# Optimization experiments

Hardware: AMD Instinct MI355X
Metric: run time of the kernel (lower is better)

The kernel has to match this reference:

```python
import jax, jax.numpy as jnp
import numpy as np

B, C, H, W = 8, 256, 64, 64
GROUPS = 32
EPS = 1e-5


def setup_inputs() -> dict:
    key = jax.random.key(0)
    ks = jax.random.split(key, 6)
    s = 1.0 / np.sqrt(C)
    return {
        "x": jax.random.normal(ks[0], (B, C, H, W), dtype=jnp.float32),
        "gn_w": jnp.ones((C,), jnp.float32),
        "gn_b": jnp.zeros((C,), jnp.float32),
        "wq": jax.random.normal(ks[1], (C, C), jnp.float32) * s,
        "bq": jnp.zeros((C,), jnp.float32),
        "wk": jax.random.normal(ks[2], (C, C), jnp.float32) * s,
        "bk": jnp.zeros((C,), jnp.float32),
        "wv": jax.random.normal(ks[3], (C, C), jnp.float32) * s,
        "bv": jnp.zeros((C,), jnp.float32),
        "wo": jax.random.normal(ks[4], (C, C), jnp.float32) * s,
        "bo": jnp.zeros((C,), jnp.float32),
    }


def group_norm(x, w, b):
    # x: [B, C, H, W]; normalize over (C//GROUPS, H, W) per group
    Bn, Cn, Hn, Wn = x.shape
    xg = x.reshape(Bn, GROUPS, Cn // GROUPS, Hn, Wn)
    mu = jnp.mean(xg, axis=(2, 3, 4), keepdims=True)
    var = jnp.var(xg, axis=(2, 3, 4), keepdims=True)
    xn = (xg - mu) * jax.lax.rsqrt(var + EPS)
    xn = xn.reshape(Bn, Cn, Hn, Wn)
    return xn * w[None, :, None, None] + b[None, :, None, None]


def reference(x, gn_w, gn_b, wq, bq, wk, bk, wv, bv, wo, bo):
    Bn, Cn, Hn, Wn = x.shape
    h = group_norm(x, gn_w, gn_b)
    hf = h.reshape(Bn, Cn, Hn * Wn)  # [B, C, N]
    # 1x1 conv == channel matmul; produce tokens-major [B, N, C]
    q = jnp.einsum('bcn,oc->bno', hf, wq) + bq  # [B, N, C]
    k = jnp.einsum('bcn,oc->bon', hf, wk) + bk[None, :, None]  # [B, C, N]
    v = jnp.einsum('bcn,oc->bno', hf, wv) + bv  # [B, N, C]
    alpha = jnp.einsum('bnc,bcm->bnm', q, k) / jnp.sqrt(jnp.float32(Cn))
    alpha = jax.nn.softmax(alpha, axis=-1)  # [B, N, N]
    out = jnp.einsum('bnm,bmc->bnc', alpha, v)  # [B, N, C]
    out = jnp.einsum('bnc,oc->bon', out, wo) + bo[None, :, None]  # [B, C, N]
    return out.reshape(Bn, Cn, Hn, Wn) + x
```

## Files before the change

kernel.cpp:

```cpp
#include <hip/hip_runtime.h>
#include <hip/hip_bf16.h>
#include <cstdint>


typedef short short8 __attribute__((ext_vector_type(8)));
typedef float f32x16 __attribute__((ext_vector_type(16)));

__device__ __forceinline__ unsigned short f2bf(float f){
  uint32_t u = __builtin_bit_cast(uint32_t, f);
  u += 0x7FFFu + ((u >> 16) & 1u);
  return (unsigned short)(u >> 16);
}
__device__ __forceinline__ uint32_t pk2t(float a, float b){
  return (__builtin_bit_cast(uint32_t,a)>>16) | (__builtin_bit_cast(uint32_t,b)&0xFFFF0000u);
}
__device__ __forceinline__ void gload16(const void* g, void* l){
  auto gp = reinterpret_cast<uint32_t __attribute__((address_space(1)))*>(
      reinterpret_cast<uintptr_t>(g));
  auto lp = reinterpret_cast<uint32_t __attribute__((address_space(3)))*>(
      reinterpret_cast<uintptr_t>(l));
  __builtin_amdgcn_global_load_lds(gp, lp, 16, 0, 0);
}

__global__ void cvt_w_kernel(const float* wq, const float* wk, const float* wv, const float* wo,
                             ushort* wqb, ushort* wkb, ushort* wvb, ushort* wob){
  int i = blockIdx.x*256 + threadIdx.x;
  wqb[i]=f2bf(wq[i]); wkb[i]=f2bf(wk[i]); wvb[i]=f2bf(wv[i]); wob[i]=f2bf(wo[i]);
}

__global__ void gn_stats_kernel(const float* __restrict__ x, float* __restrict__ gst){
  int bg = blockIdx.x;
  const float* p = x + (size_t)bg*32768;
  float s=0.f, sq=0.f;
  for(int i=threadIdx.x;i<32768;i+=256){ float v=p[i]; s+=v; sq+=v*v; }
  #pragma unroll
  for(int o=32;o>0;o>>=1){ s+=__shfl_down(s,o); sq+=__shfl_down(sq,o); }
  __shared__ float ls[4], lq[4];
  if((threadIdx.x&63)==0){ ls[threadIdx.x>>6]=s; lq[threadIdx.x>>6]=sq; }
  __syncthreads();
  if(threadIdx.x==0){
    s=ls[0]+ls[1]+ls[2]+ls[3]; sq=lq[0]+lq[1]+lq[2]+lq[3];
    float mu=s*(1.f/32768.f);
    float var=sq*(1.f/32768.f)-mu*mu;
    gst[bg*2]=mu; gst[bg*2+1]=rsqrtf(var+1e-5f);
  }
}

__global__ void gn_apply_kernel(const float* __restrict__ x, const float* __restrict__ gw,
                                const float* __restrict__ gb, const float* __restrict__ gst,
                                ushort* __restrict__ ht){
  int nt=blockIdx.x, ct=blockIdx.y, b=blockIdx.z;
  int n0=nt*64, c0=ct*32;
  __shared__ float tile[32][65];
  __shared__ float smu[4], srs[4], sw[32], sb[32];
  int tid=threadIdx.x;
  if(tid<4){ int g=(c0>>3)+tid; smu[tid]=gst[(b*32+g)*2]; srs[tid]=gst[(b*32+g)*2+1]; }
  if(tid<32){ sw[tid]=gw[c0+tid]; sb[tid]=gb[c0+tid]; }
  __syncthreads();
  int ci=tid>>3, j0=(tid&7)*8;
  const float* xp = x + ((size_t)(b*256)+c0+ci)*4096 + n0 + j0;
  float mu=smu[ci>>3], rs=srs[ci>>3], w=sw[ci], bb=sb[ci];
  #pragma unroll
  for(int j=0;j<8;j++){ tile[ci][j0+j]=(xp[j]-mu)*rs*w+bb; }
  __syncthreads();
  int nl=tid>>2, oct=tid&3;
  union{ ushort u[8]; uint4 v; } o;
  #pragma unroll
  for(int j=0;j<8;j++) o.u[j]=f2bf(tile[oct*8+j][nl]);
  *reinterpret_cast<uint4*>(ht + ((size_t)(b*4096)+n0+nl)*256 + c0 + oct*8) = o.v;
}

__global__ __launch_bounds__(256,2) void gemm_qk(const ushort* __restrict__ A,
         const ushort* __restrict__ Bq, const ushort* __restrict__ Bk,
         ushort* __restrict__ Dq, ushort* __restrict__ Dk,
         const float* __restrict__ bq, const float* __restrict__ bk, float qscale){
  __shared__ ushort Al[128*64];
  __shared__ ushort Bql[128*64];
  __shared__ ushort Bkl[128*64];
  int m0=blockIdx.x*128, n0=blockIdx.y*128;
  int tid=threadIdx.x, w=tid>>6, lane=tid&63, ln=lane&31, hi=lane>>5;
  f32x16 aq[2][2], ak[2][2];
  #pragma unroll
  for(int a=0;a<2;a++)
    #pragma unroll
    for(int c=0;c<2;c++)
      #pragma unroll
      for(int r=0;r<16;r++){ aq[a][c][r]=0.f; ak[a][c][r]=0.f; }
  for(int kt=0;kt<4;kt++){
    __syncthreads();
    #pragma unroll
    for(int i=0;i<4;i++){
      int idx=i*256+tid; int row=idx>>3; int chs=(idx^row)&7;
      gload16(A  + (size_t)(m0+row)*256 + kt*64 + chs*8, (char*)Al  + (i*256+w*64)*16);
    }
    #pragma unroll
    for(int i=0;i<4;i++){
      int idx=i*256+tid; int row=idx>>3; int chs=(idx^row)&7;
      gload16(Bq + (size_t)(n0+row)*256 + kt*64 + chs*8, (char*)Bql + (i*256+w*64)*16);
    }
    #pragma unroll
    for(int i=0;i<4;i++){
      int idx=i*256+tid; int row=idx>>3; int chs=(idx^row)&7;
      gload16(Bk + (size_t)(n0+row)*256 + kt*64 + chs*8, (char*)Bkl + (i*256+w*64)*16);
    }
    __syncthreads();
    #pragma unroll
    for(int kk=0;kk<4;kk++){
      short8 af[2], bqf[2], bkf[2];
      #pragma unroll
      for(int t=0;t<2;t++){
        int ra=(w>>1)*64+t*32+ln; int ca=((kk*2+hi)^ra)&7;
        af[t]=*reinterpret_cast<const short8*>(Al + ra*64 + ca*8);
        int rb=(w&1)*64+t*32+ln; int cb=((kk*2+hi)^rb)&7;
        bqf[t]=*reinterpret_cast<const short8*>(Bql + rb*64 + cb*8);
        bkf[t]=*reinterpret_cast<const short8*>(Bkl + rb*64 + cb*8);
      }
      #pragma unroll
      for(int ti=0;ti<2;ti++)
        #pragma unroll
        for(int tj=0;tj<2;tj++){
          aq[ti][tj]=__builtin_amdgcn_mfma_f32_32x32x16_bf16(af[ti],bqf[tj],aq[ti][tj],0,0,0);
          ak[ti][tj]=__builtin_amdgcn_mfma_f32_32x32x16_bf16(af[ti],bkf[tj],ak[ti][tj],0,0,0);
        }
    }
  }
  #pragma unroll
  for(int ti=0;ti<2;ti++){
    #pragma unroll
    for(int tj=0;tj<2;tj++){
      int col=n0+(w&1)*64+tj*32+ln;
      float bqc=bq[col], bkc=bk[col];
      #pragma unroll
      for(int r=0;r<16;r++){
        int row=m0+(w>>1)*64+ti*32+(r&3)+8*(r>>2)+4*hi;
        Dq[(size_t)row*256+col]=f2bf((aq[ti][tj][r]+bqc)*qscale);
        Dk[(size_t)row*256+col]=f2bf(ak[ti][tj][r]+bkc);
      }
    }
  }
}

__global__ __launch_bounds__(256,2) void gemm_vt(const ushort* __restrict__ A, const ushort* __restrict__ Bm,
         ushort* __restrict__ D, const float* __restrict__ bias){
  __shared__ ushort Al[128*64];
  __shared__ ushort Bl[128*64];
  int m0=blockIdx.x*128, n0=blockIdx.y*128;
  int tid=threadIdx.x, w=tid>>6, lane=tid&63, ln=lane&31, hi=lane>>5;
  f32x16 acc[2][2];
  #pragma unroll
  for(int a=0;a<2;a++)
    #pragma unroll
    for(int c=0;c<2;c++)
      #pragma unroll
      for(int r=0;r<16;r++) acc[a][c][r]=0.f;
  for(int kt=0;kt<4;kt++){
    __syncthreads();
    #pragma unroll
    for(int i=0;i<4;i++){
      int idx=i*256+tid; int row=idx>>3; int chs=(idx^row)&7;
      gload16(A + (size_t)(m0+row)*256 + kt*64 + chs*8, (char*)Al + (i*256+w*64)*16);
    }
    #pragma unroll
    for(int i=0;i<4;i++){
      int idx=i*256+tid; int row=idx>>3; int chs=(idx^row)&7;
      gload16(Bm + (size_t)(n0+row)*256 + kt*64 + chs*8, (char*)Bl + (i*256+w*64)*16);
    }
    __syncthreads();
    #pragma unroll
    for(int kk=0;kk<4;kk++){
      short8 af[2], bfr[2];
      #pragma unroll
      for(int t=0;t<2;t++){
        int ra=(w>>1)*64+t*32+ln; int ca=((kk*2+hi)^ra)&7;
        af[t]=*reinterpret_cast<const short8*>(Al + ra*64 + ca*8);
        int rb=(w&1)*64+t*32+ln; int cb=((kk*2+hi)^rb)&7;
        bfr[t]=*reinterpret_cast<const short8*>(Bl + rb*64 + cb*8);
      }
      #pragma unroll
      for(int ti=0;ti<2;ti++)
        #pragma unroll
        for(int tj=0;tj<2;tj++)
          acc[ti][tj]=__builtin_amdgcn_mfma_f32_32x32x16_bf16(af[ti],bfr[tj],acc[ti][tj],0,0,0);
    }
  }
  #pragma unroll
  for(int ti=0;ti<2;ti++){
    #pragma unroll
    for(int tj=0;tj<2;tj++){
      int col=n0+(w&1)*64+tj*32+ln;
      #pragma unroll
      for(int r=0;r<16;r++){
        int row=m0+(w>>1)*64+ti*32+(r&3)+8*(r>>2)+4*hi;
        D[(size_t)row*32768+col]=f2bf(acc[ti][tj][r]+bias[row]);
      }
    }
  }
}

__global__ __launch_bounds__(512,2) void attn_kernel(
    const ushort* __restrict__ qb, const ushort* __restrict__ kb,
    const ushort* __restrict__ vtb, const ushort* __restrict__ wob,
    const float* __restrict__ bo, const float* __restrict__ x,
    float* __restrict__ out){
  __shared__ ushort smem[2][32768];
  __shared__ float ml[8][2][32];
  float* exch = reinterpret_cast<float*>(&smem[0][0]);
  int tid=threadIdx.x, w=tid>>6, lane=tid&63, ln=lane&31, hi=lane>>5;
  int qg=w&3, h=w>>2;
  int b=blockIdx.y, n0=blockIdx.x*128+qg*32;
  int n=n0+ln;
  short8 qf[16];
  {
    const ushort* qrow = qb + ((size_t)(b*4096)+n)*256 + hi*8;
    #pragma unroll
    for(int kc=0;kc<16;kc++) qf[kc]=*reinterpret_cast<const short8*>(qrow+kc*16);
  }
  f32x16 oacc[8];
  #pragma unroll
  for(int i=0;i<8;i++)
    #pragma unroll
    for(int r=0;r<16;r++) oacc[i][r]=0.f;
  float M=-3.0e38f, L=0.f;
  const ushort* kbp = kb + (size_t)b*4096*256;
  const ushort* vbp = vtb + (size_t)b*4096;

  auto stage=[&](int t1, int bufi){
    char* Kd=(char*)&smem[bufi][0];
    char* Vd=(char*)&smem[bufi][16384];
    #pragma unroll
    for(int i=0;i<4;i++){
      int idx=i*512+tid; int row=idx>>5, ch=idx&31;
      int chs=(ch&24)|((ch^row)&7);
      gload16(kbp + (size_t)(t1*64+row)*256 + chs*8, Kd + (i*512+w*64)*16);
    }
    #pragma unroll
    for(int i=0;i<4;i++){
      int idx=i*512+tid; int row=idx>>3; int chs=(idx^row)&7;
      gload16(vbp + (size_t)row*32768 + t1*64 + chs*8, Vd + (i*512+w*64)*16);
    }
  };

  stage(0, 0);

  for(int t=0;t<64;t++){
    int cur=t&1;
    if(t<63){
      stage(t+1, cur^1);
      asm volatile("s_waitcnt vmcnt(8)" ::: "memory");
    } else {
      asm volatile("s_waitcnt vmcnt(0)" ::: "memory");
    }
    asm volatile("s_barrier" ::: "memory");
    const ushort* kBase=&smem[cur][0];
    const ushort* vBase=&smem[cur][16384];
    f32x16 s;
    #pragma unroll
    for(int r=0;r<16;r++) s[r]=0.f;
    int kr=h*32+ln;
    const ushort* klr = kBase + kr*256;
    #pragma unroll
    for(int kc=0;kc<16;kc++){
      int cw=kc*2+hi; int chs=(cw&24)|((cw^kr)&7);
      short8 a=*reinterpret_cast<const short8*>(klr+chs*8);
      s=__builtin_amdgcn_mfma_f32_32x32x16_bf16(a,qf[kc],s,0,0,0);
    }
    float tmax=fmaxf(fmaxf(fmaxf(s[0],s[1]),fmaxf(s[2],s[3])),
                     fmaxf(fmaxf(s[4],s[5]),fmaxf(s[6],s[7])));
    float tmax2=fmaxf(fmaxf(fmaxf(s[8],s[9]),fmaxf(s[10],s[11])),
                      fmaxf(fmaxf(s[12],s[13]),fmaxf(s[14],s[15])));
    tmax=fmaxf(tmax,tmax2);
    tmax=fmaxf(tmax,__shfl_xor(tmax,32));
    if(__any(tmax > M + 8.f)){
      float Mn=fmaxf(M,tmax);
      float sc=exp2f(M-Mn);
      L*=sc;
      #pragma unroll
      for(int i=0;i<8;i++)
        #pragma unroll
        for(int r=0;r<16;r++) oacc[i][r]*=sc;
      M=Mn;
    }
    float p[16]; float ts=0.f;
    #pragma unroll
    for(int r=0;r<16;r++){ p[r]=exp2f(s[r]-M); ts+=p[r]; }
    ts+=__shfl_xor(ts,32);
    L+=ts;
    short8 pa[2];
    #pragma unroll
    for(int ks=0;ks<2;ks++){
      uint32_t c01=pk2t(p[ks*8+0],p[ks*8+1]);
      uint32_t c23=pk2t(p[ks*8+2],p[ks*8+3]);
      uint32_t c45=pk2t(p[ks*8+4],p[ks*8+5]);
      uint32_t c67=pk2t(p[ks*8+6],p[ks*8+7]);
      uint32_t x01=(uint32_t)__shfl_xor((int)c01,32), x23=(uint32_t)__shfl_xor((int)c23,32);
      uint32_t x45=(uint32_t)__shfl_xor((int)c45,32), x67=(uint32_t)__shfl_xor((int)c67,32);
      union{ uint32_t u[4]; short8 v; } r_;
      r_.u[0]= hi? x45:c01;
      r_.u[1]= hi? x67:c23;
      r_.u[2]= hi? c45:x01;
      r_.u[3]= hi? c67:x23;
      pa[ks]=r_.v;
    }
    #pragma unroll
    for(int ct=0;ct<8;ct++){
      int c=ct*32+ln;
      const ushort* vlr = vBase + c*64;
      #pragma unroll
      for(int ks=0;ks<2;ks++){
        int cw=h*4+ks*2+hi; int chs=cw^(c&7);
        short8 a=*reinterpret_cast<const short8*>(vlr+chs*8);
        oacc[ct]=__builtin_amdgcn_mfma_f32_32x32x16_bf16(a,pa[ks],oacc[ct],0,0,0);
      }
    }
    asm volatile("s_barrier" ::: "memory");
  }
  __syncthreads();
  if(hi==0){ ml[w][0][ln]=M; ml[w][1][ln]=L; }
  __syncthreads();
  float Mp=ml[w^4][0][ln], Lp=ml[w^4][1][ln];
  float Mt=fmaxf(M,Mp);
  float fo=exp2f(M-Mt), fpp=exp2f(Mp-Mt);
  float g=fo/(fo*L+fpp*Lp);
  #pragma unroll
  for(int i=0;i<8;i++)
    #pragma unroll
    for(int r=0;r<16;r++) oacc[i][r]*=g;
  short8 obf[16];
  #pragma unroll
  for(int cb=0;cb<4;cb++){
    __syncthreads();
    float* ex=exch + w*2048;
    #pragma unroll
    for(int u=0;u<2;u++){
      int ct=cb*2+u;
      #pragma unroll
      for(int r=0;r<16;r++){
        int cl=u*32+(r&3)+8*(r>>2)+4*hi;
        ex[cl*32+ln]=oacc[ct][r];
      }
    }
    __syncthreads();
    const float* exq=exch + (w^4)*2048;
    #pragma unroll
    for(int u=0;u<2;u++){
      int ct=cb*2+u;
      #pragma unroll
      for(int r=0;r<16;r++){
        int cl=u*32+(r&3)+8*(r>>2)+4*hi;
        oacc[ct][r]+=exq[cl*32+ln];
      }
    }
    #pragma unroll
    for(int kq=0;kq<4;kq++){
      int ct=cb*2+(kq>>1); int rb=(kq&1)*8;
      uint32_t c01=pk2t(oacc[ct][rb+0],oacc[ct][rb+1]);
      uint32_t c23=pk2t(oacc[ct][rb+2],oacc[ct][rb+3]);
      uint32_t c45=pk2t(oacc[ct][rb+4],oacc[ct][rb+5]);
      uint32_t c67=pk2t(oacc[ct][rb+6],oacc[ct][rb+7]);
      uint32_t x01=(uint32_t)__shfl_xor((int)c01,32), x23=(uint32_t)__shfl_xor((int)c23,32);
      uint32_t x45=(uint32_t)__shfl_xor((int)c45,32), x67=(uint32_t)__shfl_xor((int)c67,32);
      union{ uint32_t u[4]; short8 v; } r_;
      r_.u[0]= hi? x45:c01;
      r_.u[1]= hi? x67:c23;
      r_.u[2]= hi? c45:x01;
      r_.u[3]= hi? c67:x23;
      obf[cb*4+kq]=r_.v;
    }
  }
  #pragma unroll
  for(int cot=0;cot<4;cot++){
    f32x16 d;
    #pragma unroll
    for(int r=0;r<16;r++) d[r]=0.f;
    int coa=h*128+cot*32+ln;
    const ushort* wr=wob+(size_t)coa*256+hi*8;
    #pragma unroll
    for(int kbv=0;kbv<16;kbv++){
      short8 a=*reinterpret_cast<const short8*>(wr+kbv*16);
      d=__builtin_amdgcn_mfma_f32_32x32x16_bf16(a,obf[kbv],d,0,0,0);
    }
    #pragma unroll
    for(int r=0;r<16;r++){
      int co=h*128+cot*32+(r&3)+8*(r>>2)+4*hi;
      size_t oi=((size_t)(b*256)+co)*4096 + n0+ln;
      out[oi]=d[r]+bo[co]+x[oi];
    }
  }
}

extern "C" void kernel_launch(void* const* d_in, const int* in_sizes, int n_in,
                              void* d_out, int out_size, void* d_ws, size_t ws_size,
                              hipStream_t stream){
  const float* x   =(const float*)d_in[0];
  const float* gw  =(const float*)d_in[1];
  const float* gb  =(const float*)d_in[2];
  const float* wq  =(const float*)d_in[3];
  const float* bq  =(const float*)d_in[4];
  const float* wk  =(const float*)d_in[5];
  const float* bk  =(const float*)d_in[6];
  const float* wv  =(const float*)d_in[7];
  const float* bv  =(const float*)d_in[8];
  const float* wo  =(const float*)d_in[9];
  const float* bo  =(const float*)d_in[10];
  float* out=(float*)d_out;
  char* ws=(char*)d_ws;
  const size_t SZ = (size_t)32768*256*2;
  ushort* ht =(ushort*)(ws);
  ushort* qb =(ushort*)(ws+SZ);
  ushort* kb2=(ushort*)(ws+2*SZ);
  ushort* vtb=(ushort*)(ws+3*SZ);
  ushort* wqb=(ushort*)(ws+4*SZ);
  ushort* wkb=(ushort*)(ws+4*SZ+131072);
  ushort* wvb=(ushort*)(ws+4*SZ+262144);
  ushort* wob=(ushort*)(ws+4*SZ+393216);
  float*  gst=(float*) (ws+4*SZ+524288);

  cvt_w_kernel<<<256,256,0,stream>>>(wq,wk,wv,wo,wqb,wkb,wvb,wob);
  gn_stats_kernel<<<256,256,0,stream>>>(x,gst);
  gn_apply_kernel<<<dim3(64,8,8),256,0,stream>>>(x,gw,gb,gst,ht);
  gemm_qk<<<dim3(256,2),256,0,stream>>>(ht,wqb,wkb,qb,kb2,bq,bk,0.090168439f);
  gemm_vt<<<dim3(2,256),256,0,stream>>>(wvb,ht,vtb,bv);
  attn_kernel<<<dim3(32,8),512,0,stream>>>(qb,kb2,vtb,wob,bo,x,out);
}
```

Baseline: 362.5 us.

## Split GN stats into two passes, vectorize loads, precompute attention LDS pointers

Group-norm statistics now run as two kernels: 2048 blocks compute partial sums with float4 loads, then a single block combines them. This replaces the old 256-block strided loop and gives more parallelism. gn_apply reads x with float4 loads. The attention main loop is unrolled by two with per-buffer precomputed swizzled LDS pointers, which removes index arithmetic from the inner loop at the cost of an extra kernel launch and more registers.

```diff
diff --git a/kernel.cpp b/kernel.cpp
--- a/kernel.cpp
+++ b/kernel.cpp
@@ -21,6 +21,8 @@
       reinterpret_cast<uintptr_t>(l));
   __builtin_amdgcn_global_load_lds(gp, lp, 16, 0, 0);
 }
+__device__ __forceinline__ float xmax32(float x){ return fmaxf(x, __shfl_xor(x,32)); }
+__device__ __forceinline__ float xsum32(float x){ return x + __shfl_xor(x,32); }
 
 __global__ void cvt_w_kernel(const float* wq, const float* wk, const float* wv, const float* wo,
                              ushort* wqb, ushort* wkb, ushort* wvb, ushort* wob){
@@ -28,22 +30,34 @@
   wqb[i]=f2bf(wq[i]); wkb[i]=f2bf(wk[i]); wvb[i]=f2bf(wv[i]); wob[i]=f2bf(wo[i]);
 }
 
-__global__ void gn_stats_kernel(const float* __restrict__ x, float* __restrict__ gst){
-  int bg = blockIdx.x;
-  const float* p = x + (size_t)bg*32768;
+__global__ void gn_stats1_kernel(const float* __restrict__ x, float* __restrict__ part){
+  int blk = blockIdx.x;
+  const float* p = x + (size_t)(blk>>3)*32768 + (blk&7)*4096;
   float s=0.f, sq=0.f;
-  for(int i=threadIdx.x;i<32768;i+=256){ float v=p[i]; s+=v; sq+=v*v; }
+  #pragma unroll
+  for(int j=0;j<4;j++){
+    float4 v = *reinterpret_cast<const float4*>(p + threadIdx.x*16 + j*4);
+    s += v.x+v.y+v.z+v.w;
+    sq += v.x*v.x+v.y*v.y+v.z*v.z+v.w*v.w;
+  }
   #pragma unroll
   for(int o=32;o>0;o>>=1){ s+=__shfl_down(s,o); sq+=__shfl_down(sq,o); }
   __shared__ float ls[4], lq[4];
   if((threadIdx.x&63)==0){ ls[threadIdx.x>>6]=s; lq[threadIdx.x>>6]=sq; }
   __syncthreads();
   if(threadIdx.x==0){
-    s=ls[0]+ls[1]+ls[2]+ls[3]; sq=lq[0]+lq[1]+lq[2]+lq[3];
-    float mu=s*(1.f/32768.f);
-    float var=sq*(1.f/32768.f)-mu*mu;
-    gst[bg*2]=mu; gst[bg*2+1]=rsqrtf(var+1e-5f);
-  }
+    part[blk*2]  =ls[0]+ls[1]+ls[2]+ls[3];
+    part[blk*2+1]=lq[0]+lq[1]+lq[2]+lq[3];
+  }
+}
+__global__ void gn_stats2_kernel(const float* __restrict__ part, float* __restrict__ gst){
+  int bg = threadIdx.x;
+  float s=0.f, sq=0.f;
+  #pragma unroll
+  for(int j=0;j<8;j++){ s+=part[(bg*8+j)*2]; sq+=part[(bg*8+j)*2+1]; }
+  float mu=s*(1.f/32768.f);
+  float var=sq*(1.f/32768.f)-mu*mu;
+  gst[bg*2]=mu; gst[bg*2+1]=rsqrtf(var+1e-5f);
 }
 
 __global__ void gn_apply_kernel(const float* __restrict__ x, const float* __restrict__ gw,
@@ -60,8 +74,12 @@
   int ci=tid>>3, j0=(tid&7)*8;
   const float* xp = x + ((size_t)(b*256)+c0+ci)*4096 + n0 + j0;
   float mu=smu[ci>>3], rs=srs[ci>>3], w=sw[ci], bb=sb[ci];
-  #pragma unroll
-  for(int j=0;j<8;j++){ tile[ci][j0+j]=(xp[j]-mu)*rs*w+bb; }
+  float4 va=*reinterpret_cast<const float4*>(xp);
+  float4 vb=*reinterpret_cast<const float4*>(xp+4);
+  tile[ci][j0+0]=(va.x-mu)*rs*w+bb; tile[ci][j0+1]=(va.y-mu)*rs*w+bb;
+  tile[ci][j0+2]=(va.z-mu)*rs*w+bb; tile[ci][j0+3]=(va.w-mu)*rs*w+bb;
+  tile[ci][j0+4]=(vb.x-mu)*rs*w+bb; tile[ci][j0+5]=(vb.y-mu)*rs*w+bb;
+  tile[ci][j0+6]=(vb.z-mu)*rs*w+bb; tile[ci][j0+7]=(vb.w-mu)*rs*w+bb;
   __syncthreads();
   int nl=tid>>2, oct=tid&3;
   union{ ushort u[8]; uint4 v; } o;
@@ -224,6 +242,19 @@
   const ushort* kbp = kb + (size_t)b*4096*256;
   const ushort* vbp = vtb + (size_t)b*4096;
 
+  int kr=h*32+ln;
+  const ushort* kT[2][4];
+  const ushort* vT[2][2];
+  #pragma unroll
+  for(int bb=0;bb<2;bb++){
+    #pragma unroll
+    for(int q=0;q<4;q++)
+      kT[bb][q] = &smem[bb][0] + kr*256 + ((((2*q+hi))^kr)&7)*8;
+    #pragma unroll
+    for(int ks=0;ks<2;ks++)
+      vT[bb][ks] = &smem[bb][16384] + ln*64 + (((h*4+ks*2+hi)^ln)&7)*8;
+  }
+
   auto stage=[&](int t1, int bufi){
     char* Kd=(char*)&smem[bufi][0];
     char* Vd=(char*)&smem[bufi][16384];
@@ -242,78 +273,75 @@
 
   stage(0, 0);
 
-  for(int t=0;t<64;t++){
-    int cur=t&1;
-    if(t<63){
-      stage(t+1, cur^1);
-      asm volatile("s_waitcnt vmcnt(8)" ::: "memory");
-    } else {
-      asm volatile("s_waitcnt vmcnt(0)" ::: "memory");
-    }
-    asm volatile("s_barrier" ::: "memory");
-    const ushort* kBase=&smem[cur][0];
-    const ushort* vBase=&smem[cur][16384];
-    f32x16 s;
-    #pragma unroll
-    for(int r=0;r<16;r++) s[r]=0.f;
-    int kr=h*32+ln;
-    const ushort* klr = kBase + kr*256;
-    #pragma unroll
-    for(int kc=0;kc<16;kc++){
-      int cw=kc*2+hi; int chs=(cw&24)|((cw^kr)&7);
-      short8 a=*reinterpret_cast<const short8*>(klr+chs*8);
-      s=__builtin_amdgcn_mfma_f32_32x32x16_bf16(a,qf[kc],s,0,0,0);
-    }
-    float tmax=fmaxf(fmaxf(fmaxf(s[0],s[1]),fmaxf(s[2],s[3])),
-                     fmaxf(fmaxf(s[4],s[5]),fmaxf(s[6],s[7])));
-    float tmax2=fmaxf(fmaxf(fmaxf(s[8],s[9]),fmaxf(s[10],s[11])),
-                      fmaxf(fmaxf(s[12],s[13]),fmaxf(s[14],s[15])));
-    tmax=fmaxf(tmax,tmax2);
-    tmax=fmaxf(tmax,__shfl_xor(tmax,32));
-    if(__any(tmax > M + 8.f)){
-      float Mn=fmaxf(M,tmax);
-      float sc=exp2f(M-Mn);
-      L*=sc;
-      #pragma unroll
-      for(int i=0;i<8;i++)
-        #pragma unroll
-        for(int r=0;r<16;r++) oacc[i][r]*=sc;
-      M=Mn;
-    }
-    float p[16]; float ts=0.f;
-    #pragma unroll
-    for(int r=0;r<16;r++){ p[r]=exp2f(s[r]-M); ts+=p[r]; }
-    ts+=__shfl_xor(ts,32);
-    L+=ts;
-    short8 pa[2];
-    #pragma unroll
-    for(int ks=0;ks<2;ks++){
-      uint32_t c01=pk2t(p[ks*8+0],p[ks*8+1]);
-      uint32_t c23=pk2t(p[ks*8+2],p[ks*8+3]);
-      uint32_t c45=pk2t(p[ks*8+4],p[ks*8+5]);
-      uint32_t c67=pk2t(p[ks*8+6],p[ks*8+7]);
-      uint32_t x01=(uint32_t)__shfl_xor((int)c01,32), x23=(uint32_t)__shfl_xor((int)c23,32);
-      uint32_t x45=(uint32_t)__shfl_xor((int)c45,32), x67=(uint32_t)__shfl_xor((int)c67,32);
-      union{ uint32_t u[4]; short8 v; } r_;
-      r_.u[0]= hi? x45:c01;
-      r_.u[1]= hi? x67:c23;
-      r_.u[2]= hi? c45:x01;
-      r_.u[3]= hi? c67:x23;
-      pa[ks]=r_.v;
-    }
-    #pragma unroll
-    for(int ct=0;ct<8;ct++){
-      int c=ct*32+ln;
-      const ushort* vlr = vBase + c*64;
-      #pragma unroll
-      for(int ks=0;ks<2;ks++){
-        int cw=h*4+ks*2+hi; int chs=cw^(c&7);
-        short8 a=*reinterpret_cast<const short8*>(vlr+chs*8);
-        oacc[ct]=__builtin_amdgcn_mfma_f32_32x32x16_bf16(a,pa[ks],oacc[ct],0,0,0);
-      }
-    }
-    asm volatile("s_barrier" ::: "memory");
-  }
+#define ATTN_STEP(T_, CUR_) {                                                  \
+    if((T_)<63){                                                               \
+      stage((T_)+1, (CUR_)^1);                                                 \
+      asm volatile("s_waitcnt vmcnt(8)" ::: "memory");                         \
+    } else {                                                                   \
+      asm volatile("s_waitcnt vmcnt(0)" ::: "memory");                         \
+    }                                                                          \
+    asm volatile("s_barrier" ::: "memory");                                    \
+    f32x16 s;                                                                  \
+    _Pragma("unroll")                                                          \
+    for(int r=0;r<16;r++) s[r]=0.f;                                            \
+    _Pragma("unroll")                                                          \
+    for(int kc=0;kc<16;kc++){                                                  \
+      short8 a=*reinterpret_cast<const short8*>(kT[CUR_][kc&3] + ((2*kc)&24)*8); \
+      s=__builtin_amdgcn_mfma_f32_32x32x16_bf16(a,qf[kc],s,0,0,0);             \
+    }                                                                          \
+    float tmax=fmaxf(fmaxf(fmaxf(s[0],s[1]),fmaxf(s[2],s[3])),                 \
+                     fmaxf(fmaxf(s[4],s[5]),fmaxf(s[6],s[7])));                \
+    float tmax2=fmaxf(fmaxf(fmaxf(s[8],s[9]),fmaxf(s[10],s[11])),              \
+                      fmaxf(fmaxf(s[12],s[13]),fmaxf(s[14],s[15])));           \
+    tmax=xmax32(fmaxf(tmax,tmax2));                                            \
+    if(__any(tmax > M + 8.f)){                                                 \
+      float Mn=fmaxf(M,tmax);                                                  \
+      float sc=exp2f(M-Mn);                                                    \
+      L*=sc;                                                                   \
+      _Pragma("unroll")                                                        \
+      for(int i=0;i<8;i++)                                                     \
+        _Pragma("unroll")                                                      \
+        for(int r=0;r<16;r++) oacc[i][r]*=sc;                                  \
+      M=Mn;                                                                    \
+    }                                                                          \
+    float p[16]; float ts=0.f;                                                 \
+    _Pragma("unroll")                                                          \
+    for(int r=0;r<16;r++){ p[r]=exp2f(s[r]-M); ts+=p[r]; }                     \
+    L+=xsum32(ts);                                                             \
+    short8 pa[2];                                                              \
+    _Pragma("unroll")                                                          \
+    for(int ks=0;ks<2;ks++){                                                   \
+      uint32_t c01=pk2t(p[ks*8+0],p[ks*8+1]);                                  \
+      uint32_t c23=pk2t(p[ks*8+2],p[ks*8+3]);                                  \
+      uint32_t c45=pk2t(p[ks*8+4],p[ks*8+5]);                                  \
+      uint32_t c67=pk2t(p[ks*8+6],p[ks*8+7]);                                  \
+      uint32_t x01=(uint32_t)__shfl_xor((int)c01,32), x23=(uint32_t)__shfl_xor((int)c23,32); \
+      uint32_t x45=(uint32_t)__shfl_xor((int)c45,32), x67=(uint32_t)__shfl_xor((int)c67,32); \
+      union{ uint32_t u[4]; short8 v; } r_;                                    \
+      r_.u[0]= hi? x45:c01;                                                    \
+      r_.u[1]= hi? x67:c23;                                                    \
+      r_.u[2]= hi? c45:x01;                                                    \
+      r_.u[3]= hi? c67:x23;                                                    \
+      pa[ks]=r_.v;                                                             \
+    }                                                                          \
+    _Pragma("unroll")                                                          \
+    for(int ct=0;ct<8;ct++){                                                   \
+      _Pragma("unroll")                                                        \
+      for(int ks=0;ks<2;ks++){                                                 \
+        short8 a=*reinterpret_cast<const short8*>(vT[CUR_][ks] + ct*2048);     \
+        oacc[ct]=__builtin_amdgcn_mfma_f32_32x32x16_bf16(a,pa[ks],oacc[ct],0,0,0); \
+      }                                                                        \
+    }                                                                          \
+    asm volatile("s_barrier" ::: "memory");                                    \
+  }
+
+  for(int tt=0;tt<32;tt++){
+    int t0=tt*2;
+    ATTN_STEP(t0, 0);
+    ATTN_STEP(t0+1, 1);
+  }
+#undef ATTN_STEP
+
   __syncthreads();
   if(hi==0){ ml[w][0][ln]=M; ml[w][1][ln]=L; }
   __syncthreads();
@@ -414,9 +442,11 @@
   ushort* wvb=(ushort*)(ws+4*SZ+262144);
   ushort* wob=(ushort*)(ws+4*SZ+393216);
   float*  gst=(float*) (ws+4*SZ+524288);
+  float*  part=(float*)(ws+4*SZ+524288+2048);
 
   cvt_w_kernel<<<256,256,0,stream>>>(wq,wk,wv,wo,wqb,wkb,wvb,wob);
-  gn_stats_kernel<<<256,256,0,stream>>>(x,gst);
+  gn_stats1_kernel<<<2048,256,0,stream>>>(x,part);
+  gn_stats2_kernel<<<1,256,0,stream>>>(part,gst);
   gn_apply_kernel<<<dim3(64,8,8),256,0,stream>>>(x,gw,gb,gst,ht);
   gemm_qk<<<dim3(256,2),256,0,stream>>>(ht,wqb,wkb,qb,kb2,bq,bk,0.090168439f);
   gemm_vt<<<dim3(2,256),256,0,stream>>>(wvb,ht,vtb,bv);
```

Result: slower. 459.6 us (+26.8%).

## Shrink attention blocks to 64 queries, split K/V staging, parallelize group-norm stats

Applied to the files above, without the earlier changes.

The attention kernel now uses 256-thread blocks over 64 queries each, with a grid of 512 blocks remapped so batches interleave. The old double buffer holding K and V together becomes single K and V buffers, each refilled as soon as its compute phase ends. This doubles the block count and cuts LDS per block, at the cost of extra barriers and less prefetch lead. Group-norm statistics are split into a 2048-block partial-sum pass plus a tiny reduction kernel. Loads in the stats and apply kernels are vectorized to float4.

```diff
diff --git a/kernel.cpp b/kernel.cpp
--- a/kernel.cpp
+++ b/kernel.cpp
@@ -21,6 +21,8 @@
       reinterpret_cast<uintptr_t>(l));
   __builtin_amdgcn_global_load_lds(gp, lp, 16, 0, 0);
 }
+__device__ __forceinline__ float xmax32(float x){ return fmaxf(x, __shfl_xor(x,32)); }
+__device__ __forceinline__ float xsum32(float x){ return x + __shfl_xor(x,32); }
 
 __global__ void cvt_w_kernel(const float* wq, const float* wk, const float* wv, const float* wo,
                              ushort* wqb, ushort* wkb, ushort* wvb, ushort* wob){
@@ -28,22 +30,34 @@
   wqb[i]=f2bf(wq[i]); wkb[i]=f2bf(wk[i]); wvb[i]=f2bf(wv[i]); wob[i]=f2bf(wo[i]);
 }
 
-__global__ void gn_stats_kernel(const float* __restrict__ x, float* __restrict__ gst){
-  int bg = blockIdx.x;
-  const float* p = x + (size_t)bg*32768;
+__global__ void gn_stats1_kernel(const float* __restrict__ x, float* __restrict__ part){
+  int blk = blockIdx.x;
+  const float* p = x + (size_t)(blk>>3)*32768 + (blk&7)*4096;
   float s=0.f, sq=0.f;
-  for(int i=threadIdx.x;i<32768;i+=256){ float v=p[i]; s+=v; sq+=v*v; }
+  #pragma unroll
+  for(int j=0;j<4;j++){
+    float4 v = *reinterpret_cast<const float4*>(p + threadIdx.x*16 + j*4);
+    s += v.x+v.y+v.z+v.w;
+    sq += v.x*v.x+v.y*v.y+v.z*v.z+v.w*v.w;
+  }
   #pragma unroll
   for(int o=32;o>0;o>>=1){ s+=__shfl_down(s,o); sq+=__shfl_down(sq,o); }
   __shared__ float ls[4], lq[4];
   if((threadIdx.x&63)==0){ ls[threadIdx.x>>6]=s; lq[threadIdx.x>>6]=sq; }
   __syncthreads();
   if(threadIdx.x==0){
-    s=ls[0]+ls[1]+ls[2]+ls[3]; sq=lq[0]+lq[1]+lq[2]+lq[3];
-    float mu=s*(1.f/32768.f);
-    float var=sq*(1.f/32768.f)-mu*mu;
-    gst[bg*2]=mu; gst[bg*2+1]=rsqrtf(var+1e-5f);
-  }
+    part[blk*2]  =ls[0]+ls[1]+ls[2]+ls[3];
+    part[blk*2+1]=lq[0]+lq[1]+lq[2]+lq[3];
+  }
+}
+__global__ void gn_stats2_kernel(const float* __restrict__ part, float* __restrict__ gst){
+  int bg = threadIdx.x;
+  float s=0.f, sq=0.f;
+  #pragma unroll
+  for(int j=0;j<8;j++){ s+=part[(bg*8+j)*2]; sq+=part[(bg*8+j)*2+1]; }
+  float mu=s*(1.f/32768.f);
+  float var=sq*(1.f/32768.f)-mu*mu;
+  gst[bg*2]=mu; gst[bg*2+1]=rsqrtf(var+1e-5f);
 }
 
 __global__ void gn_apply_kernel(const float* __restrict__ x, const float* __restrict__ gw,
@@ -60,8 +74,12 @@
   int ci=tid>>3, j0=(tid&7)*8;
   const float* xp = x + ((size_t)(b*256)+c0+ci)*4096 + n0 + j0;
   float mu=smu[ci>>3], rs=srs[ci>>3], w=sw[ci], bb=sb[ci];
-  #pragma unroll
-  for(int j=0;j<8;j++){ tile[ci][j0+j]=(xp[j]-mu)*rs*w+bb; }
+  float4 va=*reinterpret_cast<const float4*>(xp);
+  float4 vb=*reinterpret_cast<const float4*>(xp+4);
+  tile[ci][j0+0]=(va.x-mu)*rs*w+bb; tile[ci][j0+1]=(va.y-mu)*rs*w+bb;
+  tile[ci][j0+2]=(va.z-mu)*rs*w+bb; tile[ci][j0+3]=(va.w-mu)*rs*w+bb;
+  tile[ci][j0+4]=(vb.x-mu)*rs*w+bb; tile[ci][j0+5]=(vb.y-mu)*rs*w+bb;
+  tile[ci][j0+6]=(vb.z-mu)*rs*w+bb; tile[ci][j0+7]=(vb.w-mu)*rs*w+bb;
   __syncthreads();
   int nl=tid>>2, oct=tid&3;
   union{ ushort u[8]; uint4 v; } o;
@@ -197,17 +215,21 @@
   }
 }
 
-__global__ __launch_bounds__(512,2) void attn_kernel(
+__global__ __launch_bounds__(256,2) void attn_kernel(
     const ushort* __restrict__ qb, const ushort* __restrict__ kb,
     const ushort* __restrict__ vtb, const ushort* __restrict__ wob,
     const float* __restrict__ bo, const float* __restrict__ x,
     float* __restrict__ out){
-  __shared__ ushort smem[2][32768];
-  __shared__ float ml[8][2][32];
-  float* exch = reinterpret_cast<float*>(&smem[0][0]);
+  __shared__ ushort Kl[64*256];
+  __shared__ ushort Vl[256*64];
+  __shared__ float ml[4][2][32];
+  float* exch = reinterpret_cast<float*>(Kl);
   int tid=threadIdx.x, w=tid>>6, lane=tid&63, ln=lane&31, hi=lane>>5;
-  int qg=w&3, h=w>>2;
-  int b=blockIdx.y, n0=blockIdx.x*128+qg*32;
+  int qg=w&1, h=w>>1;
+  int bid=blockIdx.x;
+  int cid=(bid&7)*64 + (bid>>3);
+  int b=cid>>6, nt=cid&63;
+  int n0=nt*64+qg*32;
   int n=n0+ln;
   short8 qf[16];
   {
@@ -224,52 +246,45 @@
   const ushort* kbp = kb + (size_t)b*4096*256;
   const ushort* vbp = vtb + (size_t)b*4096;
 
-  auto stage=[&](int t1, int bufi){
-    char* Kd=(char*)&smem[bufi][0];
-    char* Vd=(char*)&smem[bufi][16384];
-    #pragma unroll
-    for(int i=0;i<4;i++){
-      int idx=i*512+tid; int row=idx>>5, ch=idx&31;
+  auto stageK=[&](int t1){
+    #pragma unroll
+    for(int i=0;i<8;i++){
+      int idx=i*256+tid; int row=idx>>5, ch=idx&31;
       int chs=(ch&24)|((ch^row)&7);
-      gload16(kbp + (size_t)(t1*64+row)*256 + chs*8, Kd + (i*512+w*64)*16);
-    }
-    #pragma unroll
-    for(int i=0;i<4;i++){
-      int idx=i*512+tid; int row=idx>>3; int chs=(idx^row)&7;
-      gload16(vbp + (size_t)row*32768 + t1*64 + chs*8, Vd + (i*512+w*64)*16);
+      gload16(kbp + (size_t)(t1*64+row)*256 + chs*8, (char*)Kl + (i*256+w*64)*16);
     }
   };
-
-  stage(0, 0);
+  auto stageV=[&](int t1){
+    #pragma unroll
+    for(int i=0;i<8;i++){
+      int idx=i*256+tid; int row=idx>>3; int chs=(idx^row)&7;
+      gload16(vbp + (size_t)row*32768 + t1*64 + chs*8, (char*)Vl + (i*256+w*64)*16);
+    }
+  };
+
+  stageK(0); stageV(0);
 
   for(int t=0;t<64;t++){
-    int cur=t&1;
-    if(t<63){
-      stage(t+1, cur^1);
-      asm volatile("s_waitcnt vmcnt(8)" ::: "memory");
-    } else {
-      asm volatile("s_waitcnt vmcnt(0)" ::: "memory");
-    }
+    asm volatile("s_waitcnt vmcnt(8)" ::: "memory");
     asm volatile("s_barrier" ::: "memory");
-    const ushort* kBase=&smem[cur][0];
-    const ushort* vBase=&smem[cur][16384];
     f32x16 s;
     #pragma unroll
     for(int r=0;r<16;r++) s[r]=0.f;
     int kr=h*32+ln;
-    const ushort* klr = kBase + kr*256;
+    const ushort* klr = Kl + kr*256;
     #pragma unroll
     for(int kc=0;kc<16;kc++){
       int cw=kc*2+hi; int chs=(cw&24)|((cw^kr)&7);
       short8 a=*reinterpret_cast<const short8*>(klr+chs*8);
       s=__builtin_amdgcn_mfma_f32_32x32x16_bf16(a,qf[kc],s,0,0,0);
     }
+    asm volatile("s_barrier" ::: "memory");
+    if(t<63) stageK(t+1);
     float tmax=fmaxf(fmaxf(fmaxf(s[0],s[1]),fmaxf(s[2],s[3])),
                      fmaxf(fmaxf(s[4],s[5]),fmaxf(s[6],s[7])));
     float tmax2=fmaxf(fmaxf(fmaxf(s[8],s[9]),fmaxf(s[10],s[11])),
                       fmaxf(fmaxf(s[12],s[13]),fmaxf(s[14],s[15])));
-    tmax=fmaxf(tmax,tmax2);
-    tmax=fmaxf(tmax,__shfl_xor(tmax,32));
+    tmax=xmax32(fmaxf(tmax,tmax2));
     if(__any(tmax > M + 8.f)){
       float Mn=fmaxf(M,tmax);
       float sc=exp2f(M-Mn);
@@ -283,8 +298,7 @@
     float p[16]; float ts=0.f;
     #pragma unroll
     for(int r=0;r<16;r++){ p[r]=exp2f(s[r]-M); ts+=p[r]; }
-    ts+=__shfl_xor(ts,32);
-    L+=ts;
+    L+=xsum32(ts);
     short8 pa[2];
     #pragma unroll
     for(int ks=0;ks<2;ks++){
@@ -301,10 +315,13 @@
       r_.u[3]= hi? c67:x23;
       pa[ks]=r_.v;
     }
+    if(t<63){ asm volatile("s_waitcnt vmcnt(8)" ::: "memory"); }
+    else    { asm volatile("s_waitcnt vmcnt(0)" ::: "memory"); }
+    asm volatile("s_barrier" ::: "memory");
     #pragma unroll
     for(int ct=0;ct<8;ct++){
       int c=ct*32+ln;
-      const ushort* vlr = vBase + c*64;
+      const ushort* vlr = Vl + c*64;
       #pragma unroll
       for(int ks=0;ks<2;ks++){
         int cw=h*4+ks*2+hi; int chs=cw^(c&7);
@@ -313,11 +330,12 @@
       }
     }
     asm volatile("s_barrier" ::: "memory");
+    if(t<63) stageV(t+1);
   }
   __syncthreads();
   if(hi==0){ ml[w][0][ln]=M; ml[w][1][ln]=L; }
   __syncthreads();
-  float Mp=ml[w^4][0][ln], Lp=ml[w^4][1][ln];
+  float Mp=ml[w^2][0][ln], Lp=ml[w^2][1][ln];
   float Mt=fmaxf(M,Mp);
   float fo=exp2f(M-Mt), fpp=exp2f(Mp-Mt);
   float g=fo/(fo*L+fpp*Lp);
@@ -340,7 +358,7 @@
       }
     }
     __syncthreads();
-    const float* exq=exch + (w^4)*2048;
+    const float* exq=exch + (w^2)*2048;
     #pragma unroll
     for(int u=0;u<2;u++){
       int ct=cb*2+u;
@@ -414,11 +432,13 @@
   ushort* wvb=(ushort*)(ws+4*SZ+262144);
   ushort* wob=(ushort*)(ws+4*SZ+393216);
   float*  gst=(float*) (ws+4*SZ+524288);
+  float*  part=(float*)(ws+4*SZ+524288+2048);
 
   cvt_w_kernel<<<256,256,0,stream>>>(wq,wk,wv,wo,wqb,wkb,wvb,wob);
-  gn_stats_kernel<<<256,256,0,stream>>>(x,gst);
+  gn_stats1_kernel<<<2048,256,0,stream>>>(x,part);
+  gn_stats2_kernel<<<1,256,0,stream>>>(part,gst);
   gn_apply_kernel<<<dim3(64,8,8),256,0,stream>>>(x,gw,gb,gst,ht);
   gemm_qk<<<dim3(256,2),256,0,stream>>>(ht,wqb,wkb,qb,kb2,bq,bk,0.090168439f);
   gemm_vt<<<dim3(2,256),256,0,stream>>>(wvb,ht,vtb,bv);
-  attn_kernel<<<dim3(32,8),512,0,stream>>>(qb,kb2,vtb,wob,bo,x,out);
-}
+  attn_kernel<<<512,256,0,stream>>>(qb,kb2,vtb,wob,bo,x,out);
+}
```

Measured after the change: 342.2 us. 1.06x faster.
